# Kernel optimization log

Hardware: AMD Instinct MI355X
Metric: run time of the kernel (lower is better)

## Reference

```python
import jax, jax.numpy as jnp
import numpy as np

ALPHA = 0.5
N_NODES = 100000
N_EDGES = 1600000
D_IN = 128
D_OUT = 128


def setup_inputs() -> dict:
    key = jax.random.key(0)
    k1, k2, k3, k4, k5, k6 = jax.random.split(key, 6)
    x = jax.random.normal(k1, (N_NODES, D_IN), dtype=jnp.float32)
    edge_index = jax.random.randint(k2, (2, N_EDGES), 0, N_NODES, dtype=jnp.int64)
    # torch Linear default init: U(-1/sqrt(fan_in), 1/sqrt(fan_in)); scale similar here
    s = 1.0 / np.sqrt(D_IN)
    W_src = jax.random.uniform(k3, (D_OUT, D_IN), jnp.float32, -s, s)
    b_src = jax.random.uniform(k4, (D_OUT,), jnp.float32, -s, s)
    W_dst = jax.random.uniform(k5, (D_OUT, D_IN), jnp.float32, -s, s)
    b_dst = jax.random.uniform(k6, (D_OUT,), jnp.float32, -s, s)
    return {"x": x, "edge_index": edge_index, "W_src": W_src, "b_src": b_src,
            "W_dst": W_dst, "b_dst": b_dst}


def _inv_sqrt(deg):
    # deg^{-1/2} with inf -> 0 (isolated nodes)
    return jnp.where(deg > 0, jax.lax.rsqrt(jnp.maximum(deg, 1e-30)), 0.0)


def reference(x, edge_index, W_src, b_src, W_dst, b_dst):
    n = x.shape[0]
    row, col = edge_index[0], edge_index[1]
    ones = jnp.ones(row.shape[0], dtype=x.dtype)
    # degrees of directed adjacency A[row, col] = 1
    deg_out = jax.ops.segment_sum(ones, row, num_segments=n)  # row sums
    deg_in = jax.ops.segment_sum(ones, col, num_segments=n)   # col sums
    # D_out^{-1/2} A D_in^{-1/2} edge weights; transpose norm yields the SAME weights
    w = _inv_sqrt(deg_out)[row] * _inv_sqrt(deg_in)[col]      # [E]
    # adj_norm @ x : aggregate sources (col) into destinations (row)
    agg_fwd = jax.ops.segment_sum(w[:, None] * x[col], row, num_segments=n)  # [N, D_IN]
    # adj_t_norm @ x : aggregate destinations (row) into sources (col)
    agg_bwd = jax.ops.segment_sum(w[:, None] * x[row], col, num_segments=n)  # [N, D_IN]
    out = ALPHA * (agg_fwd @ W_src.T + b_src) + (1.0 - ALPHA) * (agg_bwd @ W_dst.T + b_dst)
    return out
```

## Files before the change

kernel.cpp:

```cpp
#include <hip/hip_runtime.h>
#include <stdint.h>

#define D 128
#define CE 2048
#define CAP 5120

typedef __attribute__((ext_vector_type(8))) __bf16 bf16x8;
typedef __attribute__((ext_vector_type(4))) float floatx4;

union FragU { uint4 u; bf16x8 b; };

__device__ __forceinline__ float bf16_lo(uint32_t u) { return __uint_as_float(u << 16); }
__device__ __forceinline__ float bf16_hi(uint32_t u) { return __uint_as_float(u & 0xffff0000u); }
__device__ __forceinline__ uint16_t f32_to_bf16(float f) {
    uint32_t u = __float_as_uint(f);
    uint32_t r = u + 0x7fffu + ((u >> 16) & 1u);
    return (uint16_t)(r >> 16);
}
__device__ __forceinline__ uint32_t pack2(float a, float b) {
    return (uint32_t)f32_to_bf16(a) | ((uint32_t)f32_to_bf16(b) << 16);
}

__global__ __launch_bounds__(256) void k_init(uint32_t* __restrict__ gcursor, int nb2)
{
    for (int j = threadIdx.x + blockIdx.x * 256; j < nb2; j += gridDim.x * 256)
        gcursor[j] = (uint32_t)j * CAP;
}

__global__ __launch_bounds__(256) void k_part(
    const int* __restrict__ ei, int E, int nbuk,
    uint32_t* __restrict__ gcursor, uint32_t* __restrict__ gpairs)
{
    __shared__ uint32_t cnt[1024];
    __shared__ uint32_t loff[1024];
    __shared__ uint32_t gbase[1024];
    __shared__ uint32_t spair[2 * CE];
    __shared__ uint16_t sbid[2 * CE];
    __shared__ uint32_t ssum[256];
    int nb2 = 2 * nbuk;
    for (int j = threadIdx.x; j < nb2; j += 256) cnt[j] = 0;
    __syncthreads();
    int base = blockIdx.x * CE;
    int lim = min(CE, E - base);
    for (int i = threadIdx.x; i < lim; i += 256) {
        int r = ei[base + i];
        int c = ei[E + base + i];
        atomicAdd(&cnt[r >> 8], 1u);
        atomicAdd(&cnt[nbuk + (c >> 8)], 1u);
    }
    __syncthreads();
    uint32_t v0 = 0, v1 = 0, v2 = 0, v3 = 0;
    int b0 = threadIdx.x * 4;
    if (b0 < nb2)     v0 = cnt[b0];
    if (b0 + 1 < nb2) v1 = cnt[b0 + 1];
    if (b0 + 2 < nb2) v2 = cnt[b0 + 2];
    if (b0 + 3 < nb2) v3 = cnt[b0 + 3];
    uint32_t tsum = v0 + v1 + v2 + v3;
    ssum[threadIdx.x] = tsum;
    __syncthreads();
    for (int off = 1; off < 256; off <<= 1) {
        uint32_t t = (threadIdx.x >= (unsigned)off) ? ssum[threadIdx.x - off] : 0u;
        __syncthreads();
        ssum[threadIdx.x] += t;
        __syncthreads();
    }
    uint32_t run = ssum[threadIdx.x] - tsum;
    if (b0 < nb2)     loff[b0]     = run;
    if (b0 + 1 < nb2) loff[b0 + 1] = run + v0;
    if (b0 + 2 < nb2) loff[b0 + 2] = run + v0 + v1;
    if (b0 + 3 < nb2) loff[b0 + 3] = run + v0 + v1 + v2;
    __syncthreads();
    for (int j = threadIdx.x; j < nb2; j += 256) {
        uint32_t c2 = cnt[j];
        gbase[j] = c2 ? atomicAdd(&gcursor[j], c2) : 0u;
        cnt[j] = loff[j];
    }
    __syncthreads();
    for (int i = threadIdx.x; i < lim; i += 256) {
        int r = ei[base + i];
        int c = ei[E + base + i];
        int bf = r >> 8;
        uint32_t sf = atomicAdd(&cnt[bf], 1u);
        spair[sf] = ((uint32_t)c << 8) | (uint32_t)(r & 255);
        sbid[sf] = (uint16_t)bf;
        int bb = nbuk + (c >> 8);
        uint32_t sb = atomicAdd(&cnt[bb], 1u);
        spair[sb] = ((uint32_t)r << 8) | (uint32_t)(c & 255);
        sbid[sb] = (uint16_t)bb;
    }
    __syncthreads();
    int total = 2 * lim;
    for (int s2 = threadIdx.x; s2 < total; s2 += 256) {
        int b = sbid[s2];
        gpairs[gbase[b] + ((uint32_t)s2 - loff[b])] = spair[s2];
    }
}

__global__ __launch_bounds__(256) void k_build(
    const uint32_t* __restrict__ gpairs, const uint32_t* __restrict__ gcursor,
    int nbuk, int N,
    int* __restrict__ edata, uint32_t* __restrict__ ptrg, uint32_t* __restrict__ degg,
    float* __restrict__ inv_o, float* __restrict__ inv_i)
{
    __shared__ uint32_t hist[256], cur[256], ssum[256];
    __shared__ int sdata[CAP];
    int b = blockIdx.x;
    int dir = (b >= nbuk) ? 1 : 0;
    int node0 = (b - dir * nbuk) << 8;
    uint32_t base = (uint32_t)b * CAP;
    uint32_t cnt_b = gcursor[b] - base;
    hist[threadIdx.x] = 0;
    __syncthreads();
    for (uint32_t i = threadIdx.x; i < cnt_b; i += 256)
        atomicAdd(&hist[gpairs[base + i] & 255u], 1u);
    __syncthreads();
    uint32_t h = hist[threadIdx.x];
    ssum[threadIdx.x] = h;
    __syncthreads();
    for (int off = 1; off < 256; off <<= 1) {
        uint32_t t = (threadIdx.x >= (unsigned)off) ? ssum[threadIdx.x - off] : 0u;
        __syncthreads();
        ssum[threadIdx.x] += t;
        __syncthreads();
    }
    uint32_t excl = ssum[threadIdx.x] - h;
    cur[threadIdx.x] = excl;
    int n = node0 + threadIdx.x;
    if (n < N) {
        ptrg[dir * N + n] = base + excl;
        degg[dir * N + n] = h;
        float iv = h ? rsqrtf((float)h) : 0.0f;
        if (dir == 0) inv_o[n] = iv; else inv_i[n] = iv;
    }
    __syncthreads();
    for (uint32_t i = threadIdx.x; i < cnt_b; i += 256) {
        uint32_t e = gpairs[base + i];
        uint32_t pos = atomicAdd(&cur[e & 255u], 1u);
        sdata[pos] = (int)(e >> 8);
    }
    __syncthreads();
    uint32_t c4 = cnt_b & ~3u;
    for (uint32_t i = 4 * threadIdx.x; i < c4; i += 1024) {
        *(int4*)&edata[base + i] = *(const int4*)&sdata[i];
    }
    for (uint32_t i = c4 + threadIdx.x; i < cnt_b; i += 256)
        edata[base + i] = sdata[i];
}

__global__ __launch_bounds__(256) void k_mm(
    const float* __restrict__ x,
    const float* __restrict__ Wsrc, const float* __restrict__ Wdst,
    const float* __restrict__ inv_o, const float* __restrict__ inv_i,
    uint32_t* __restrict__ u2, uint32_t* __restrict__ v2, int N)
{
    __shared__ uint4 sWf[2048];
    const int lane = threadIdx.x & 63;
    const int m16 = lane & 15;
    const int quad = lane >> 4;
    const int mat = blockIdx.x & 1;
    uint32_t* outb = mat ? v2 : u2;
    const float* inv = mat ? inv_o : inv_i;
    const float* Wm = mat ? Wdst : Wsrc;

    {
        uint32_t* sW32 = (uint32_t*)sWf;
        for (int idx = threadIdx.x; idx < 8192; idx += 256) {
            int slot = idx >> 2, j2 = idx & 3;
            int ct = slot >> 8, ks = (slot >> 6) & 3, qd = (slot >> 4) & 3, mm = slot & 15;
            const float2 w = *(const float2*)(Wm + (ct * 16 + mm) * 128 + ks * 32 + qd * 8 + 2 * j2);
            sW32[idx] = pack2(0.5f * w.x, 0.5f * w.y);
        }
    }
    __syncthreads();

    const int ntiles = (N + 15) >> 4;
    const int wslot = (blockIdx.x >> 1) * 4 + (threadIdx.x >> 6);
    const int nslot = (gridDim.x >> 1) * 4;

    for (int t = wslot; t < ntiles; t += nslot) {
        int node = t * 16 + m16;
        int rowA = node < N ? node : N - 1;
        const float4* xr = (const float4*)(x + (long)rowA * 128);
        bf16x8 Xf[4];
        #pragma unroll
        for (int ks = 0; ks < 4; ++ks) {
            float4 p0 = xr[ks * 8 + quad * 2];
            float4 p1 = xr[ks * 8 + quad * 2 + 1];
            FragU f;
            f.u.x = pack2(p0.x, p0.y);
            f.u.y = pack2(p0.z, p0.w);
            f.u.z = pack2(p1.x, p1.y);
            f.u.w = pack2(p1.z, p1.w);
            Xf[ks] = f.b;
        }
        float iv = mat ? inv_o[rowA] : inv_i[rowA];
        bool ok = (node < N);
        #pragma unroll
        for (int ct = 0; ct < 8; ++ct) {
            floatx4 acc = {};
            #pragma unroll
            for (int ks = 0; ks < 4; ++ks) {
                FragU wf; wf.u = sWf[ct * 256 + ks * 64 + lane];
                acc = __builtin_amdgcn_mfma_f32_16x16x32_bf16(wf.b, Xf[ks], acc, 0, 0, 0);
            }
            if (ok) {
                uint2 val;
                val.x = pack2(acc[0] * iv, acc[1] * iv);
                val.y = pack2(acc[2] * iv, acc[3] * iv);
                *(uint2*)(outb + (long)node * 64 + ct * 8 + quad * 2) = val;
            }
        }
    }
}

__global__ __launch_bounds__(256) void k_gather(
    const uint32_t* __restrict__ u2, const uint32_t* __restrict__ v2,
    const int* __restrict__ edata,
    const uint32_t* __restrict__ ptrg, const uint32_t* __restrict__ degg,
    const float* __restrict__ inv_out, const float* __restrict__ inv_in,
    const float* __restrict__ bsrc, const float* __restrict__ bdst,
    float* __restrict__ out, int N, int nStart, int nEnd)
{
    const int lane = threadIdx.x & 63;
    const int h = lane >> 5;
    const int j = lane & 31;
    const float4 bs = *(const float4*)(bsrc + 4 * j);
    const float4 bd = *(const float4*)(bdst + 4 * j);
    const int wid = blockIdx.x * 4 + (threadIdx.x >> 6);
    const int nw = gridDim.x * 4;

    for (int node = nStart + wid; node < nEnd; node += nw) {
        uint32_t s0 = ptrg[node],     d0 = degg[node];
        uint32_t s1 = ptrg[N + node], d1 = degg[N + node];
        float io = inv_out[node], ii = inv_in[node];

        float f0 = 0, f1 = 0, f2 = 0, f3 = 0;
        {
            uint32_t k = 0;
            for (; k + 8 <= d0; k += 8) {
                int i0 = edata[s0 + k     + h];
                int i1 = edata[s0 + k + 2 + h];
                int i2 = edata[s0 + k + 4 + h];
                int i3 = edata[s0 + k + 6 + h];
                uint2 p0 = *(const uint2*)(u2 + (long)i0 * 64 + 2 * j);
                uint2 p1 = *(const uint2*)(u2 + (long)i1 * 64 + 2 * j);
                uint2 p2 = *(const uint2*)(u2 + (long)i2 * 64 + 2 * j);
                uint2 p3 = *(const uint2*)(u2 + (long)i3 * 64 + 2 * j);
                f0 += bf16_lo(p0.x) + bf16_lo(p1.x) + bf16_lo(p2.x) + bf16_lo(p3.x);
                f1 += bf16_hi(p0.x) + bf16_hi(p1.x) + bf16_hi(p2.x) + bf16_hi(p3.x);
                f2 += bf16_lo(p0.y) + bf16_lo(p1.y) + bf16_lo(p2.y) + bf16_lo(p3.y);
                f3 += bf16_hi(p0.y) + bf16_hi(p1.y) + bf16_hi(p2.y) + bf16_hi(p3.y);
            }
            for (; k + 2 <= d0; k += 2) {
                int i0 = edata[s0 + k + h];
                uint2 p = *(const uint2*)(u2 + (long)i0 * 64 + 2 * j);
                f0 += bf16_lo(p.x); f1 += bf16_hi(p.x);
                f2 += bf16_lo(p.y); f3 += bf16_hi(p.y);
            }
            if (k < d0 && h == 0) {
                int i0 = edata[s0 + k];
                uint2 p = *(const uint2*)(u2 + (long)i0 * 64 + 2 * j);
                f0 += bf16_lo(p.x); f1 += bf16_hi(p.x);
                f2 += bf16_lo(p.y); f3 += bf16_hi(p.y);
            }
        }

        float g0 = 0, g1 = 0, g2 = 0, g3 = 0;
        {
            uint32_t k = 0;
            for (; k + 8 <= d1; k += 8) {
                int i0 = edata[s1 + k     + h];
                int i1 = edata[s1 + k + 2 + h];
                int i2 = edata[s1 + k + 4 + h];
                int i3 = edata[s1 + k + 6 + h];
                uint2 p0 = *(const uint2*)(v2 + (long)i0 * 64 + 2 * j);
                uint2 p1 = *(const uint2*)(v2 + (long)i1 * 64 + 2 * j);
                uint2 p2 = *(const uint2*)(v2 + (long)i2 * 64 + 2 * j);
                uint2 p3 = *(const uint2*)(v2 + (long)i3 * 64 + 2 * j);
                g0 += bf16_lo(p0.x) + bf16_lo(p1.x) + bf16_lo(p2.x) + bf16_lo(p3.x);
                g1 += bf16_hi(p0.x) + bf16_hi(p1.x) + bf16_hi(p2.x) + bf16_hi(p3.x);
                g2 += bf16_lo(p0.y) + bf16_lo(p1.y) + bf16_lo(p2.y) + bf16_lo(p3.y);
                g3 += bf16_hi(p0.y) + bf16_hi(p1.y) + bf16_hi(p2.y) + bf16_hi(p3.y);
            }
            for (; k + 2 <= d1; k += 2) {
                int i0 = edata[s1 + k + h];
                uint2 p = *(const uint2*)(v2 + (long)i0 * 64 + 2 * j);
                g0 += bf16_lo(p.x); g1 += bf16_hi(p.x);
                g2 += bf16_lo(p.y); g3 += bf16_hi(p.y);
            }
            if (k < d1 && h == 0) {
                int i0 = edata[s1 + k];
                uint2 p = *(const uint2*)(v2 + (long)i0 * 64 + 2 * j);
                g0 += bf16_lo(p.x); g1 += bf16_hi(p.x);
                g2 += bf16_lo(p.y); g3 += bf16_hi(p.y);
            }
        }

        f0 += __shfl_xor(f0, 32); f1 += __shfl_xor(f1, 32);
        f2 += __shfl_xor(f2, 32); f3 += __shfl_xor(f3, 32);
        g0 += __shfl_xor(g0, 32); g1 += __shfl_xor(g1, 32);
        g2 += __shfl_xor(g2, 32); g3 += __shfl_xor(g3, 32);

        if (h == 0) {
            float4 o;
            o.x = io * f0 + ii * g0 + 0.5f * (bs.x + bd.x);
            o.y = io * f1 + ii * g1 + 0.5f * (bs.y + bd.y);
            o.z = io * f2 + ii * g2 + 0.5f * (bs.z + bd.z);
            o.w = io * f3 + ii * g3 + 0.5f * (bs.w + bd.w);
            *(float4*)(out + (long)node * 128 + 4 * j) = o;
        }
    }
}

extern "C" void kernel_launch(void* const* d_in, const int* in_sizes, int n_in,
                              void* d_out, int out_size, void* d_ws, size_t ws_size,
                              hipStream_t stream) {
    const int N = in_sizes[0] / D;
    const int E = in_sizes[1] / 2;
    const int nbuk = (N + 255) >> 8;
    const int nb2 = 2 * nbuk;

    const float* x    = (const float*)d_in[0];
    const int*   ei   = (const int*)d_in[1];
    const float* Wsrc = (const float*)d_in[2];
    const float* bsrc = (const float*)d_in[3];
    const float* Wdst = (const float*)d_in[4];
    const float* bdst = (const float*)d_in[5];

    char* ws = (char*)d_ws;
    size_t off = 0;
    uint32_t* gcur   = (uint32_t*)(ws + off); off += 1024 * 4;
    float*    inv_o  = (float*)(ws + off);    off += (size_t)N * 4;
    float*    inv_i  = (float*)(ws + off);    off += (size_t)N * 4;
    uint32_t* ptrg   = (uint32_t*)(ws + off); off += (size_t)2 * N * 4;
    uint32_t* degg   = (uint32_t*)(ws + off); off += (size_t)2 * N * 4;
    uint32_t* gpairs = (uint32_t*)(ws + off); off += (size_t)nb2 * CAP * 4;
    int*      edata  = (int*)(ws + off);      off += (size_t)nb2 * CAP * 4;
    uint32_t* u2     = (uint32_t*)(ws + off); off += (size_t)N * 64 * 4;
    uint32_t* v2     = (uint32_t*)(ws + off); off += (size_t)N * 64 * 4;

    k_init<<<4, 256, 0, stream>>>(gcur, nb2);

    k_part<<<(E + CE - 1) / CE, 256, 0, stream>>>(ei, E, nbuk, gcur, gpairs);

    k_build<<<nb2, 256, 0, stream>>>(gpairs, gcur, nbuk, N,
                                     edata, ptrg, degg, inv_o, inv_i);

    k_mm<<<2048, 256, 0, stream>>>(x, Wsrc, Wdst, inv_o, inv_i, u2, v2, N);

    k_gather<<<2048, 256, 0, stream>>>(u2, v2, edata, ptrg, degg,
                                       inv_o, inv_i, bsrc, bdst,
                                       (float*)d_out, N, 0, N);
}
```

Before: 318.5 us.

## Prefetch next x tile in k_mm, use wave-shuffle scans, enlarge partition chunk

The matmul kernel now software-pipelines its loop: it loads the next tile's x rows and inverse degree into registers before running the MFMA work on the current tile, so load latency is hidden. Its grid is also halved so each wave handles more tiles. The block-wide prefix scans in k_part and k_build move from a shared-memory Hillis-Steele loop with many barriers to a wavefront shuffle scan plus a small cross-wave combine. The partition chunk CE is doubled, which halves the k_part block count and the global cursor atomics, but doubles its shared memory use and may lower occupancy.

```diff
diff --git a/kernel.cpp b/kernel.cpp
--- a/kernel.cpp
+++ b/kernel.cpp
@@ -2,7 +2,7 @@
 #include <stdint.h>
 
 #define D 128
-#define CE 2048
+#define CE 4096
 #define CAP 5120
 
 typedef __attribute__((ext_vector_type(8))) __bf16 bf16x8;
@@ -21,6 +21,25 @@
     return (uint32_t)f32_to_bf16(a) | ((uint32_t)f32_to_bf16(b) << 16);
 }
 
+__device__ __forceinline__ uint32_t block_excl_scan_256(
+    uint32_t val, uint32_t* tmp4, int tid)
+{
+    int lane = tid & 63, wid = tid >> 6;
+    uint32_t inc = val;
+    #pragma unroll
+    for (int off = 1; off < 64; off <<= 1) {
+        uint32_t t = __shfl_up(inc, off, 64);
+        if (lane >= off) inc += t;
+    }
+    if (lane == 63) tmp4[wid] = inc;
+    __syncthreads();
+    uint32_t wofs = 0;
+    #pragma unroll
+    for (int w = 0; w < 4; ++w) wofs += (w < wid) ? tmp4[w] : 0u;
+    __syncthreads();
+    return wofs + inc - val;
+}
+
 __global__ __launch_bounds__(256) void k_init(uint32_t* __restrict__ gcursor, int nb2)
 {
     for (int j = threadIdx.x + blockIdx.x * 256; j < nb2; j += gridDim.x * 256)
@@ -36,7 +55,7 @@
     __shared__ uint32_t gbase[1024];
     __shared__ uint32_t spair[2 * CE];
     __shared__ uint16_t sbid[2 * CE];
-    __shared__ uint32_t ssum[256];
+    __shared__ uint32_t stmp[4];
     int nb2 = 2 * nbuk;
     for (int j = threadIdx.x; j < nb2; j += 256) cnt[j] = 0;
     __syncthreads();
@@ -56,15 +75,7 @@
     if (b0 + 2 < nb2) v2 = cnt[b0 + 2];
     if (b0 + 3 < nb2) v3 = cnt[b0 + 3];
     uint32_t tsum = v0 + v1 + v2 + v3;
-    ssum[threadIdx.x] = tsum;
-    __syncthreads();
-    for (int off = 1; off < 256; off <<= 1) {
-        uint32_t t = (threadIdx.x >= (unsigned)off) ? ssum[threadIdx.x - off] : 0u;
-        __syncthreads();
-        ssum[threadIdx.x] += t;
-        __syncthreads();
-    }
-    uint32_t run = ssum[threadIdx.x] - tsum;
+    uint32_t run = block_excl_scan_256(tsum, stmp, threadIdx.x);
     if (b0 < nb2)     loff[b0]     = run;
     if (b0 + 1 < nb2) loff[b0 + 1] = run + v0;
     if (b0 + 2 < nb2) loff[b0 + 2] = run + v0 + v1;
@@ -102,7 +113,7 @@
     int* __restrict__ edata, uint32_t* __restrict__ ptrg, uint32_t* __restrict__ degg,
     float* __restrict__ inv_o, float* __restrict__ inv_i)
 {
-    __shared__ uint32_t hist[256], cur[256], ssum[256];
+    __shared__ uint32_t hist[256], cur[256], stmp[4];
     __shared__ int sdata[CAP];
     int b = blockIdx.x;
     int dir = (b >= nbuk) ? 1 : 0;
@@ -115,15 +126,7 @@
         atomicAdd(&hist[gpairs[base + i] & 255u], 1u);
     __syncthreads();
     uint32_t h = hist[threadIdx.x];
-    ssum[threadIdx.x] = h;
-    __syncthreads();
-    for (int off = 1; off < 256; off <<= 1) {
-        uint32_t t = (threadIdx.x >= (unsigned)off) ? ssum[threadIdx.x - off] : 0u;
-        __syncthreads();
-        ssum[threadIdx.x] += t;
-        __syncthreads();
-    }
-    uint32_t excl = ssum[threadIdx.x] - h;
+    uint32_t excl = block_excl_scan_256(h, stmp, threadIdx.x);
     cur[threadIdx.x] = excl;
     int n = node0 + threadIdx.x;
     if (n < N) {
@@ -177,38 +180,64 @@
     const int wslot = (blockIdx.x >> 1) * 4 + (threadIdx.x >> 6);
     const int nslot = (gridDim.x >> 1) * 4;
 
-    for (int t = wslot; t < ntiles; t += nslot) {
-        int node = t * 16 + m16;
-        int rowA = node < N ? node : N - 1;
-        const float4* xr = (const float4*)(x + (long)rowA * 128);
-        bf16x8 Xf[4];
-        #pragma unroll
-        for (int ks = 0; ks < 4; ++ks) {
-            float4 p0 = xr[ks * 8 + quad * 2];
-            float4 p1 = xr[ks * 8 + quad * 2 + 1];
-            FragU f;
-            f.u.x = pack2(p0.x, p0.y);
-            f.u.y = pack2(p0.z, p0.w);
-            f.u.z = pack2(p1.x, p1.y);
-            f.u.w = pack2(p1.z, p1.w);
-            Xf[ks] = f.b;
-        }
-        float iv = mat ? inv_o[rowA] : inv_i[rowA];
-        bool ok = (node < N);
-        #pragma unroll
-        for (int ct = 0; ct < 8; ++ct) {
-            floatx4 acc = {};
+    int t = wslot;
+    if (t < ntiles) {
+        float4 P[8];
+        float ivr;
+        {
+            int node = t * 16 + m16;
+            int rowA = node < N ? node : N - 1;
+            const float4* xr = (const float4*)(x + (long)rowA * 128);
             #pragma unroll
             for (int ks = 0; ks < 4; ++ks) {
-                FragU wf; wf.u = sWf[ct * 256 + ks * 64 + lane];
-                acc = __builtin_amdgcn_mfma_f32_16x16x32_bf16(wf.b, Xf[ks], acc, 0, 0, 0);
-            }
-            if (ok) {
-                uint2 val;
-                val.x = pack2(acc[0] * iv, acc[1] * iv);
-                val.y = pack2(acc[2] * iv, acc[3] * iv);
-                *(uint2*)(outb + (long)node * 64 + ct * 8 + quad * 2) = val;
-            }
+                P[2 * ks]     = xr[ks * 8 + quad * 2];
+                P[2 * ks + 1] = xr[ks * 8 + quad * 2 + 1];
+            }
+            ivr = inv[rowA];
+        }
+        while (true) {
+            int node = t * 16 + m16;
+            bool ok = (node < N);
+            float iv = ivr;
+            bf16x8 Xf[4];
+            #pragma unroll
+            for (int ks = 0; ks < 4; ++ks) {
+                FragU f;
+                f.u.x = pack2(P[2 * ks].x,     P[2 * ks].y);
+                f.u.y = pack2(P[2 * ks].z,     P[2 * ks].w);
+                f.u.z = pack2(P[2 * ks + 1].x, P[2 * ks + 1].y);
+                f.u.w = pack2(P[2 * ks + 1].z, P[2 * ks + 1].w);
+                Xf[ks] = f.b;
+            }
+            int tn = t + nslot;
+            if (tn < ntiles) {
+                int noden = tn * 16 + m16;
+                int rowN = noden < N ? noden : N - 1;
+                const float4* xrn = (const float4*)(x + (long)rowN * 128);
+                #pragma unroll
+                for (int ks = 0; ks < 4; ++ks) {
+                    P[2 * ks]     = xrn[ks * 8 + quad * 2];
+                    P[2 * ks + 1] = xrn[ks * 8 + quad * 2 + 1];
+                }
+                ivr = inv[rowN];
+            }
+            #pragma unroll
+            for (int ct = 0; ct < 8; ++ct) {
+                floatx4 acc = {};
+                #pragma unroll
+                for (int ks = 0; ks < 4; ++ks) {
+                    FragU wf; wf.u = sWf[ct * 256 + ks * 64 + lane];
+                    acc = __builtin_amdgcn_mfma_f32_16x16x32_bf16(wf.b, Xf[ks], acc, 0, 0, 0);
+                }
+                if (ok) {
+                    uint2 val;
+                    val.x = pack2(acc[0] * iv, acc[1] * iv);
+                    val.y = pack2(acc[2] * iv, acc[3] * iv);
+                    *(uint2*)(outb + (long)node * 64 + ct * 8 + quad * 2) = val;
+                }
+            }
+            if (tn >= ntiles) break;
+            t = tn;
         }
     }
 }
@@ -346,7 +375,7 @@
     k_build<<<nb2, 256, 0, stream>>>(gpairs, gcur, nbuk, N,
                                      edata, ptrg, degg, inv_o, inv_i);
 
-    k_mm<<<2048, 256, 0, stream>>>(x, Wsrc, Wdst, inv_o, inv_i, u2, v2, N);
+    k_mm<<<1024, 256, 0, stream>>>(x, Wsrc, Wdst, inv_o, inv_i, u2, v2, N);
 
     k_gather<<<2048, 256, 0, stream>>>(u2, v2, edata, ptrg, degg,
                                        inv_o, inv_i, bsrc, bdst,
```

Result: faster. 297.3 us (-6.6%).
